# Optimization experiments

Hardware: AMD Instinct MI355X
Metric: run time of the kernel (lower is better)

## Reference

```python
import jax, jax.numpy as jnp
import numpy as np

N_NODES = 40000
N_EDGES = 320000
N_GRAPHS = 64
IN_DIM = 128
HID4 = 256   # hidden_dim * 4
OUT_DIM = 128
LN_EPS = 1e-5


def setup_inputs() -> dict:
    key = jax.random.key(0)
    ks = jax.random.split(key, 12)
    x = jax.random.normal(ks[0], (N_NODES, IN_DIM), dtype=jnp.float32)
    w = jax.random.uniform(ks[1], (N_EDGES, 4), dtype=jnp.float32)
    src = jax.random.randint(ks[2], (N_EDGES,), 0, N_NODES, dtype=jnp.int32)
    dst = jax.random.randint(ks[3], (N_EDGES,), 0, N_NODES, dtype=jnp.int32)
    graph_ids = jnp.sort(jax.random.randint(ks[4], (N_NODES,), 0, N_GRAPHS, dtype=jnp.int32))
    # parameters (no biases on GraphConv / fc1 linear)
    W1 = jax.random.normal(ks[5], (IN_DIM, HID4), dtype=jnp.float32) / np.sqrt(IN_DIM)
    fc1_W = jax.random.normal(ks[6], (IN_DIM, HID4), dtype=jnp.float32) / np.sqrt(IN_DIM)
    ln_gamma = jnp.ones((HID4,), dtype=jnp.float32)
    ln_beta = jnp.zeros((HID4,), dtype=jnp.float32)
    W2 = jax.random.normal(ks[7], (2 * HID4, HID4), dtype=jnp.float32) / np.sqrt(2 * HID4)
    W3 = jax.random.normal(ks[8], (HID4, OUT_DIM), dtype=jnp.float32) / np.sqrt(HID4)
    return {"x": x, "w": w, "W1": W1, "fc1_W": fc1_W, "ln_gamma": ln_gamma,
            "ln_beta": ln_beta, "W2": W2, "W3": W3,
            "src": src, "dst": dst, "graph_ids": graph_ids}


def _graph_conv(feat, src, dst, ew, W, out_inv_sqrt, in_inv_sqrt):
    # DGL GraphConv, norm='both', bias=False, with scalar edge_weight:
    # h = D_out^{-1/2} x ; m_e = w_e * h[src] ; agg = scatter_add(m, dst) ;
    # out = (D_in^{-1/2} agg) @ W
    h = feat * out_inv_sqrt[:, None]
    m = h[src] * ew[:, None]                       # [E, D] messages
    agg = jax.ops.segment_sum(m, dst, num_segments=N_NODES)
    return (agg * in_inv_sqrt[:, None]) @ W


def reference(x, w, W1, fc1_W, ln_gamma, ln_beta, W2, W3, src, dst, graph_ids):
    # unweighted degree normalization (DGL uses structural degrees, clamp(min=1))
    ones_e = jnp.ones((N_EDGES,), dtype=x.dtype)
    out_deg = jnp.maximum(jax.ops.segment_sum(ones_e, src, num_segments=N_NODES), 1.0)
    in_deg = jnp.maximum(jax.ops.segment_sum(ones_e, dst, num_segments=N_NODES), 1.0)
    out_inv = out_deg ** -0.5
    in_inv = in_deg ** -0.5

    ew = jnp.max(w, axis=1)                        # [E]

    x1 = jax.nn.relu(_graph_conv(x, src, dst, ew, W1, out_inv, in_inv))

    # fc1: Linear(no bias) -> LayerNorm(affine) -> ReLU
    f1 = x @ fc1_W
    mu = jnp.mean(f1, axis=-1, keepdims=True)
    var = jnp.mean((f1 - mu) ** 2, axis=-1, keepdims=True)
    f1 = (f1 - mu) * jax.lax.rsqrt(var + LN_EPS) * ln_gamma + ln_beta
    f1 = jax.nn.relu(f1)

    x1f1 = jnp.concatenate([x1, f1], axis=1)       # [N, 512]
    x2 = jax.nn.relu(_graph_conv(x1f1, src, dst, ew, W2, out_inv, in_inv))
    x3 = jax.nn.relu(_graph_conv(x2, src, dst, ew, W3, out_inv, in_inv))

    # dgl.sum_nodes over batched graph, then row-wise L2 normalize
    readout = jax.ops.segment_sum(x3, graph_ids, num_segments=N_GRAPHS)  # [G, OUT_DIM]
    norm = jnp.maximum(jnp.linalg.norm(readout, axis=1, keepdims=True), 1e-12)
    return readout / norm
```

## Files before the change

### kernel.cpp

```cpp
#include <hip/hip_runtime.h>

#define N_NODES 40000
#define M_PAD   40064
#define N_EDGES 320000
#define N_GRAPHS 64
#define IN_DIM 128
#define HID4 256
#define OUT_DIM 128
#define LN_EPS 1e-5f

typedef short  s16x8  __attribute__((ext_vector_type(8)));
typedef short  s16x4  __attribute__((ext_vector_type(4)));
typedef __bf16 bf16x8 __attribute__((ext_vector_type(8)));
typedef float  f32x4  __attribute__((ext_vector_type(4)));

__device__ __forceinline__ unsigned short f2b(float f) {
    unsigned int u = __builtin_bit_cast(unsigned int, f);
    u += 0x7fffu + ((u >> 16) & 1u);
    return (unsigned short)(u >> 16);
}
__device__ __forceinline__ float b2f(unsigned short h) {
    unsigned int u = (unsigned int)h << 16;
    return __builtin_bit_cast(float, u);
}

__device__ __forceinline__ void gll16(const unsigned short* g, short* lds_base) {
    __builtin_amdgcn_global_load_lds(
        (const __attribute__((address_space(1))) unsigned int*)g,
        (__attribute__((address_space(3))) unsigned int*)lds_base, 16, 0, 0);
}


#define XN (N_NODES * IN_DIM)
#define WN 229376
#define PREP_TOT (XN + WN + N_EDGES)

__global__ void prep_all(const float* __restrict__ x, const float* __restrict__ W1,
                         const float* __restrict__ fc1, const float* __restrict__ W2,
                         const float* __restrict__ W3, const float* __restrict__ w,
                         const int* __restrict__ src, const int* __restrict__ dst,
                         unsigned short* __restrict__ xb, unsigned short* __restrict__ W1t,
                         unsigned short* __restrict__ fc1t, unsigned short* __restrict__ W2t,
                         unsigned short* __restrict__ W3t, float* __restrict__ ew,
                         int* __restrict__ cnt_out, int* __restrict__ cnt_in) {
    int idx = blockIdx.x * 256 + threadIdx.x;
    if (idx < XN) { xb[idx] = f2b(x[idx]); return; }
    int j = idx - XN;
    if (j < 32768) { int k = j >> 8, n = j & 255; W1t[n * 128 + k] = f2b(W1[j]); return; }
    j -= 32768;
    if (j < 32768) { int k = j >> 8, n = j & 255; fc1t[n * 128 + k] = f2b(fc1[j]); return; }
    j -= 32768;
    if (j < 131072) { int k = j >> 8, n = j & 255; W2t[n * 512 + k] = f2b(W2[j]); return; }
    j -= 131072;
    if (j < 32768) { int k = j >> 7, n = j & 127; W3t[n * 256 + k] = f2b(W3[j]); return; }
    j -= 32768;
    if (j < N_EDGES) {
        float4 v = ((const float4*)w)[j];
        ew[j] = fmaxf(fmaxf(v.x, v.y), fmaxf(v.z, v.w));
        atomicAdd(&cnt_out[src[j]], 1);
        atomicAdd(&cnt_in[dst[j]], 1);
    }
}

__global__ void scan_part(const int* __restrict__ cnt, int* __restrict__ partial) {
    int b = blockIdx.x;
    int s = 0;
    for (int i = threadIdx.x; i < 1000; i += 256) s += cnt[b * 1000 + i];
#pragma unroll
    for (int m = 1; m < 64; m <<= 1) s += __shfl_xor(s, m);
    __shared__ int wsm[4];
    if ((threadIdx.x & 63) == 0) wsm[threadIdx.x >> 6] = s;
    __syncthreads();
    if (threadIdx.x == 0) partial[b] = wsm[0] + wsm[1] + wsm[2] + wsm[3];
}

__global__ void scan_final(const int* __restrict__ cnt_in, const int* __restrict__ cnt_out,
                           const int* __restrict__ partial, int* __restrict__ off,
                           float* __restrict__ out_inv, float* __restrict__ in_inv) {
    int b = blockIdx.x, tid = threadIdx.x;
    int lane = tid & 63, wv = tid >> 6;
    int pre = 0;
    for (int j = 0; j < b; ++j) pre += partial[j];
    int i = b * 1000 + tid;
    int v = (tid < 1000) ? cnt_in[i] : 0;
    int x = v;
#pragma unroll
    for (int ofs = 1; ofs < 64; ofs <<= 1) {
        int t = __shfl_up(x, ofs);
        if (lane >= ofs) x += t;
    }
    __shared__ int wsum[16];
    if (lane == 63) wsum[wv] = x;
    __syncthreads();
    if (wv == 0 && lane < 16) {
        int s = wsum[lane];
#pragma unroll
        for (int ofs = 1; ofs < 16; ofs <<= 1) {
            int t = __shfl_up(s, ofs);
            if (lane >= ofs) s += t;
        }
        wsum[lane] = s;
    }
    __syncthreads();
    int incl = pre + (wv > 0 ? wsum[wv - 1] : 0) + x;
    if (tid < 1000) {
        off[i] = incl - v;
        in_inv[i] = rsqrtf(fmaxf((float)v, 1.0f));
        out_inv[i] = rsqrtf(fmaxf((float)cnt_out[i], 1.0f));
    }
    if (b == 39 && tid == 999) off[N_NODES] = incl;
}

__global__ void csr_fill(const int* __restrict__ src, const int* __restrict__ dst,
                         const float* __restrict__ ew, const float* __restrict__ out_inv,
                         const int* __restrict__ off, int* __restrict__ cnt_in,
                         int2* __restrict__ es1, int2* __restrict__ es23) {
    int e = blockIdx.x * 256 + threadIdx.x;
    if (e >= N_EDGES) return;
    int d = dst[e];
    int slot = off[d] + atomicSub(&cnt_in[d], 1) - 1;
    int s = src[e];
    float wv = ew[e];
    es1[slot] = make_int2(s, __float_as_int(wv * out_inv[s]));
    es23[slot] = make_int2(s, __float_as_int(wv));
}


template <int D, int RELU>
__global__ void gather_nodes(const unsigned short* __restrict__ h, const int* __restrict__ off,
                             const int2* __restrict__ eg, const float* __restrict__ scale,
                             unsigned short* __restrict__ outb) {
    int n = blockIdx.x;
    int t = threadIdx.x;
    int b = off[n], e = off[n + 1];
    const unsigned int* hu = (const unsigned int*)h;
    float a0 = 0.0f, a1 = 0.0f;
    int i = b;
    for (; i + 3 < e; i += 4) {
        int2 e0 = eg[i], e1 = eg[i + 1], e2 = eg[i + 2], e3 = eg[i + 3];
        unsigned int p0 = hu[(size_t)e0.x * (D / 2) + t];
        unsigned int p1 = hu[(size_t)e1.x * (D / 2) + t];
        unsigned int p2 = hu[(size_t)e2.x * (D / 2) + t];
        unsigned int p3 = hu[(size_t)e3.x * (D / 2) + t];
        float w0 = __int_as_float(e0.y), w1 = __int_as_float(e1.y);
        float w2 = __int_as_float(e2.y), w3 = __int_as_float(e3.y);
        a0 += w0 * b2f((unsigned short)p0) + w1 * b2f((unsigned short)p1)
            + w2 * b2f((unsigned short)p2) + w3 * b2f((unsigned short)p3);
        a1 += w0 * b2f((unsigned short)(p0 >> 16)) + w1 * b2f((unsigned short)(p1 >> 16))
            + w2 * b2f((unsigned short)(p2 >> 16)) + w3 * b2f((unsigned short)(p3 >> 16));
    }
    for (; i < e; ++i) {
        int2 ee = eg[i];
        unsigned int p = hu[(size_t)ee.x * (D / 2) + t];
        float w0 = __int_as_float(ee.y);
        a0 += w0 * b2f((unsigned short)p);
        a1 += w0 * b2f((unsigned short)(p >> 16));
    }
    float sc = scale[n];
    a0 *= sc; a1 *= sc;
    if (RELU) { a0 = fmaxf(a0, 0.0f); a1 = fmaxf(a1, 0.0f); }
    unsigned int o = (unsigned int)f2b(a0) | ((unsigned int)f2b(a1) << 16);
    ((unsigned int*)outb)[(size_t)n * (D / 2) + t] = o;
}


__device__ __forceinline__ void gemm_core(short* As, short* Bs,
    const unsigned short* __restrict__ A, const unsigned short* __restrict__ A2,
    const unsigned short* __restrict__ Bt, unsigned short* __restrict__ C,
    const float* __restrict__ rowScaleC, int K1, int K2, int N,
    int relu, int scaleC, int m0, int n0) {
    int tid = threadIdx.x;
    int lane = tid & 63, wave = tid >> 6;
    int wm = (wave >> 1) * 64, wn = (wave & 1) * 64;
    int quad = lane >> 4, r16 = lane & 15;
    const int K = K1 + K2;
    f32x4 acc[4][4] = {};
    int lrow = wave * 16 + (lane >> 2);
    int kc = (lane & 3) * 8;
    short* ldsA = As + wave * 512;
    short* ldsB = Bs + wave * 512;

    for (int k0 = 0; k0 < K; k0 += 32) {
        int kk = k0 + kc;
#pragma unroll
        for (int h = 0; h < 2; ++h) {
            int r = h * 64 + lrow;
            const unsigned short* Ap = (kk < K1)
                ? A  + (size_t)(m0 + r) * K1 + kk
                : A2 + (size_t)(m0 + r) * K2 + (kk - K1);
            gll16(Ap, ldsA + h * 2048);
            gll16(Bt + (size_t)(n0 + r) * K + kk, ldsB + h * 2048);
        }
        __syncthreads();
        s16x8 af[4], bfr[4];
#pragma unroll
        for (int i = 0; i < 4; ++i)
            af[i] = *(const s16x8*)(As + (wm + i * 16 + r16) * 32 + quad * 8);
#pragma unroll
        for (int j = 0; j < 4; ++j)
            bfr[j] = *(const s16x8*)(Bs + (wn + j * 16 + r16) * 32 + quad * 8);
#pragma unroll
        for (int i = 0; i < 4; ++i)
#pragma unroll
            for (int j = 0; j < 4; ++j)
                acc[i][j] = __builtin_amdgcn_mfma_f32_16x16x32_bf16(
                    __builtin_bit_cast(bf16x8, af[i]), __builtin_bit_cast(bf16x8, bfr[j]),
                    acc[i][j], 0, 0, 0);
        __syncthreads();
    }

#pragma unroll
    for (int i = 0; i < 4; ++i) {
        int mbase = m0 + wm + i * 16 + quad * 4;
#pragma unroll
        for (int r = 0; r < 4; ++r) {
            int m = mbase + r;
            float sc = scaleC ? rowScaleC[m] : 1.0f;
#pragma unroll
            for (int j = 0; j < 4; ++j) {
                float v = acc[i][j][r] * sc;
                if (relu) v = fmaxf(v, 0.0f);
                C[(size_t)m * N + n0 + wn + j * 16 + r16] = f2b(v);
            }
        }
    }
}

template <int RELU, int SCALE_C>
__global__ __launch_bounds__(256) void gemm_mfma(
    const unsigned short* __restrict__ A, const unsigned short* __restrict__ A2,
    const unsigned short* __restrict__ Bt, unsigned short* __restrict__ C,
    const float* __restrict__ rowScaleC, int K1, int K2, int N) {
    __shared__ short As[4096];
    __shared__ short Bs[4096];
    gemm_core(As, Bs, A, A2, Bt, C, rowScaleC, K1, K2, N, RELU, SCALE_C,
              blockIdx.x * 128, blockIdx.y * 128);
}

__global__ __launch_bounds__(256) void gemm_dual(
    const unsigned short* __restrict__ A0, const unsigned short* __restrict__ B0,
    unsigned short* __restrict__ C0,
    const unsigned short* __restrict__ A1, const unsigned short* __restrict__ B1,
    unsigned short* __restrict__ C1) {
    __shared__ short As[4096];
    __shared__ short Bs[4096];
    const unsigned short* A  = blockIdx.z ? A1 : A0;
    const unsigned short* Bt = blockIdx.z ? B1 : B0;
    unsigned short* C        = blockIdx.z ? C1 : C0;
    gemm_core(As, Bs, A, A, Bt, C, nullptr, 128, 0, 256, blockIdx.z == 0, 0,
              blockIdx.x * 128, blockIdx.y * 128);
}


__global__ void ln_relu_bf16(unsigned short* __restrict__ f, const float* __restrict__ gamma,
                             const float* __restrict__ beta) {
    int row = (blockIdx.x * 256 + threadIdx.x) >> 6;
    int lane = threadIdx.x & 63;
    if (row >= N_NODES) return;
    s16x4* fr = (s16x4*)(f + (size_t)row * HID4);
    s16x4 pv = fr[lane];
    float v0 = b2f((unsigned short)pv[0]);
    float v1 = b2f((unsigned short)pv[1]);
    float v2 = b2f((unsigned short)pv[2]);
    float v3 = b2f((unsigned short)pv[3]);
    float sum = v0 + v1 + v2 + v3;
#pragma unroll
    for (int m = 1; m < 64; m <<= 1) sum += __shfl_xor(sum, m);
    float mu = sum * (1.0f / HID4);
    float d0 = v0 - mu, d1 = v1 - mu, d2 = v2 - mu, d3 = v3 - mu;
    float sq = d0 * d0 + d1 * d1 + d2 * d2 + d3 * d3;
#pragma unroll
    for (int m = 1; m < 64; m <<= 1) sq += __shfl_xor(sq, m);
    float rs = rsqrtf(sq * (1.0f / HID4) + LN_EPS);
    int c = lane * 4;
    s16x4 ov;
    ov[0] = (short)f2b(fmaxf(d0 * rs * gamma[c + 0] + beta[c + 0], 0.0f));
    ov[1] = (short)f2b(fmaxf(d1 * rs * gamma[c + 1] + beta[c + 1], 0.0f));
    ov[2] = (short)f2b(fmaxf(d2 * rs * gamma[c + 2] + beta[c + 2], 0.0f));
    ov[3] = (short)f2b(fmaxf(d3 * rs * gamma[c + 3] + beta[c + 3], 0.0f));
    fr[lane] = ov;
}


#define RO_NPB 16

__global__ void readout_sum(const unsigned short* __restrict__ x3, const int* __restrict__ gid,
                            float* __restrict__ ro) {
    int d = threadIdx.x;
    int n0 = blockIdx.x * RO_NPB;
    int n1 = n0 + RO_NPB;
    if (n1 > N_NODES) n1 = N_NODES;
    float acc = 0.0f;
    int cur = gid[n0];
    for (int n = n0; n < n1; ++n) {
        int g = gid[n];
        if (g != cur) {
            atomicAdd(&ro[cur * OUT_DIM + d], acc);
            acc = 0.0f;
            cur = g;
        }
        acc += b2f(x3[(size_t)n * OUT_DIM + d]);
    }
    atomicAdd(&ro[cur * OUT_DIM + d], acc);
}

__global__ void normalize_out(const float* __restrict__ ro, float* __restrict__ out) {
    int g = blockIdx.x;
    int d = threadIdx.x;
    float v = ro[g * OUT_DIM + d];
    float ss = v * v;
#pragma unroll
    for (int m = 1; m < 64; m <<= 1) ss += __shfl_xor(ss, m);
    __shared__ float s2[2];
    if ((d & 63) == 0) s2[d >> 6] = ss;
    __syncthreads();
    float tot = s2[0] + s2[1];
    float norm = fmaxf(sqrtf(tot), 1e-12f);
    out[g * OUT_DIM + d] = v / norm;
}


extern "C" void kernel_launch(void* const* d_in, const int* in_sizes, int n_in,
                              void* d_out, int out_size, void* d_ws, size_t ws_size,
                              hipStream_t stream) {
    const float* x    = (const float*)d_in[0];
    const float* w    = (const float*)d_in[1];
    const float* W1   = (const float*)d_in[2];
    const float* fc1W = (const float*)d_in[3];
    const float* gam  = (const float*)d_in[4];
    const float* bet  = (const float*)d_in[5];
    const float* W2   = (const float*)d_in[6];
    const float* W3   = (const float*)d_in[7];
    const int* src = (const int*)d_in[8];
    const int* dst = (const int*)d_in[9];
    const int* gid = (const int*)d_in[10];
    float* out = (float*)d_out;

    float* ws = (float*)d_ws;
    float* out_inv = ws + 0;
    float* in_inv  = ws + 40000;
    float* ew      = ws + 80000;
    int*   cnt_out = (int*)(ws + 400000);
    int*   cnt_in  = (int*)(ws + 440000);
    float* ro      = ws + 480000;
    unsigned short* W1t  = (unsigned short*)(ws + 488192);
    unsigned short* fc1t = (unsigned short*)(ws + 504576);
    unsigned short* W2t  = (unsigned short*)(ws + 520960);
    unsigned short* W3t  = (unsigned short*)(ws + 586496);
    int*   partial = (int*)(ws + 602880);
    int*   off     = (int*)(ws + 602920);
    int2*  es1     = (int2*)(ws + 642922);
    int2*  es23    = (int2*)(ws + 1282922);
    unsigned short* xb    = (unsigned short*)(ws + 1923000);
    unsigned short* Q3b   = xb;
    unsigned short* agg1b = (unsigned short*)(ws + 4487100);
    unsigned short* x2b   = agg1b;
    unsigned short* x1b   = (unsigned short*)(ws + 9615300);
    unsigned short* x3b   = x1b;
    unsigned short* f1b   = (unsigned short*)(ws + 14743500);
    unsigned short* P2b   = (unsigned short*)(ws + 19871700);

    hipMemsetAsync(cnt_out, 0, (2 * 40000 + N_GRAPHS * OUT_DIM) * sizeof(float), stream);

    prep_all<<<(PREP_TOT + 255) / 256, 256, 0, stream>>>(x, W1, fc1W, W2, W3, w, src, dst,
                                                         xb, W1t, fc1t, W2t, W3t, ew,
                                                         cnt_out, cnt_in);
    scan_part<<<40, 256, 0, stream>>>(cnt_in, partial);
    scan_final<<<40, 1024, 0, stream>>>(cnt_in, cnt_out, partial, off, out_inv, in_inv);
    csr_fill<<<(N_EDGES + 255) / 256, 256, 0, stream>>>(src, dst, ew, out_inv, off, cnt_in,
                                                        es1, es23);

    gather_nodes<IN_DIM, 0><<<N_NODES, IN_DIM / 2, 0, stream>>>(xb, off, es1, in_inv, agg1b);
    {
        dim3 grid(M_PAD / 128, HID4 / 128, 2);
        gemm_dual<<<grid, 256, 0, stream>>>(agg1b, W1t, x1b, xb, fc1t, f1b);
    }
    ln_relu_bf16<<<N_NODES / 4, 256, 0, stream>>>(f1b, gam, bet);

    {
        dim3 grid(M_PAD / 128, HID4 / 128);
        gemm_mfma<0, 1><<<grid, 256, 0, stream>>>(x1b, f1b, W2t, P2b, out_inv,
                                                  HID4, HID4, HID4);
    }
    gather_nodes<HID4, 1><<<N_NODES, HID4 / 2, 0, stream>>>(P2b, off, es23, in_inv, x2b);

    {
        dim3 grid(M_PAD / 128, OUT_DIM / 128);
        gemm_mfma<0, 1><<<grid, 256, 0, stream>>>(x2b, nullptr, W3t, Q3b, out_inv,
                                                  HID4, 0, OUT_DIM);
    }
    gather_nodes<OUT_DIM, 1><<<N_NODES, OUT_DIM / 2, 0, stream>>>(Q3b, off, es23, in_inv, x3b);

    readout_sum<<<(N_NODES + RO_NPB - 1) / RO_NPB, 128, 0, stream>>>(x3b, gid, ro);
    normalize_out<<<N_GRAPHS, 128, 0, stream>>>(ro, out);
}
```

Before: 298.3 us.

## Fuse LayerNorm into fc1 GEMM epilogue and layer-3 gather into readout

The dual GEMM now covers the full 256-column width per block with 512 threads, so the LayerNorm row statistics for fc1 can be reduced in shared memory and applied in the epilogue. This removes the separate ln_relu pass over f1. The layer-3 gather also feeds the per-graph readout directly with atomics, so x3 is never written out or re-read. The costs are fewer GEMM blocks, a single-pass variance formula (E[x²]−mu²) that can lose precision, and a gather kernel that handles 8 nodes per 64-thread block and may expose less parallelism.

```diff
diff --git a/kernel.cpp b/kernel.cpp
--- a/kernel.cpp
+++ b/kernel.cpp
@@ -10,7 +10,6 @@
 #define LN_EPS 1e-5f
 
 typedef short  s16x8  __attribute__((ext_vector_type(8)));
-typedef short  s16x4  __attribute__((ext_vector_type(4)));
 typedef __bf16 bf16x8 __attribute__((ext_vector_type(8)));
 typedef float  f32x4  __attribute__((ext_vector_type(4)));
 
@@ -164,6 +163,58 @@
 }
 
 
+#define G3_NPB 8
+
+__global__ void gather3_ro(const unsigned short* __restrict__ h, const int* __restrict__ off,
+                           const int2* __restrict__ eg, const float* __restrict__ scale,
+                           const int* __restrict__ gid, float* __restrict__ ro) {
+    int t = threadIdx.x;
+    int n0 = blockIdx.x * G3_NPB;
+    int n1 = n0 + G3_NPB;
+    if (n1 > N_NODES) n1 = N_NODES;
+    const unsigned int* hu = (const unsigned int*)h;
+    float r0 = 0.0f, r1 = 0.0f;
+    int cur = gid[n0];
+    for (int n = n0; n < n1; ++n) {
+        int g = gid[n];
+        if (g != cur) {
+            atomicAdd(&ro[cur * OUT_DIM + 2 * t], r0);
+            atomicAdd(&ro[cur * OUT_DIM + 2 * t + 1], r1);
+            r0 = r1 = 0.0f;
+            cur = g;
+        }
+        int b = off[n], e = off[n + 1];
+        float a0 = 0.0f, a1 = 0.0f;
+        int i = b;
+        for (; i + 3 < e; i += 4) {
+            int2 e0 = eg[i], e1 = eg[i + 1], e2 = eg[i + 2], e3 = eg[i + 3];
+            unsigned int p0 = hu[(size_t)e0.x * 64 + t];
+            unsigned int p1 = hu[(size_t)e1.x * 64 + t];
+            unsigned int p2 = hu[(size_t)e2.x * 64 + t];
+            unsigned int p3 = hu[(size_t)e3.x * 64 + t];
+            float w0 = __int_as_float(e0.y), w1 = __int_as_float(e1.y);
+            float w2 = __int_as_float(e2.y), w3 = __int_as_float(e3.y);
+            a0 += w0 * b2f((unsigned short)p0) + w1 * b2f((unsigned short)p1)
+                + w2 * b2f((unsigned short)p2) + w3 * b2f((unsigned short)p3);
+            a1 += w0 * b2f((unsigned short)(p0 >> 16)) + w1 * b2f((unsigned short)(p1 >> 16))
+                + w2 * b2f((unsigned short)(p2 >> 16)) + w3 * b2f((unsigned short)(p3 >> 16));
+        }
+        for (; i < e; ++i) {
+            int2 ee = eg[i];
+            unsigned int p = hu[(size_t)ee.x * 64 + t];
+            float w0 = __int_as_float(ee.y);
+            a0 += w0 * b2f((unsigned short)p);
+            a1 += w0 * b2f((unsigned short)(p >> 16));
+        }
+        float sc = scale[n];
+        r0 += fmaxf(a0 * sc, 0.0f);
+        r1 += fmaxf(a1 * sc, 0.0f);
+    }
+    atomicAdd(&ro[cur * OUT_DIM + 2 * t], r0);
+    atomicAdd(&ro[cur * OUT_DIM + 2 * t + 1], r1);
+}
+
+
 __device__ __forceinline__ void gemm_core(short* As, short* Bs,
     const unsigned short* __restrict__ A, const unsigned short* __restrict__ A2,
     const unsigned short* __restrict__ Bt, unsigned short* __restrict__ C,
@@ -237,72 +288,106 @@
               blockIdx.x * 128, blockIdx.y * 128);
 }
 
-__global__ __launch_bounds__(256) void gemm_dual(
+
+__global__ __launch_bounds__(512) void gemm_dual(
     const unsigned short* __restrict__ A0, const unsigned short* __restrict__ B0,
     unsigned short* __restrict__ C0,
     const unsigned short* __restrict__ A1, const unsigned short* __restrict__ B1,
-    unsigned short* __restrict__ C1) {
+    unsigned short* __restrict__ C1,
+    const float* __restrict__ gamma, const float* __restrict__ beta) {
     __shared__ short As[4096];
-    __shared__ short Bs[4096];
+    __shared__ short Bs[8192];
+    __shared__ float lns[128][4];
+    __shared__ float lnq[128][4];
     const unsigned short* A  = blockIdx.z ? A1 : A0;
     const unsigned short* Bt = blockIdx.z ? B1 : B0;
     unsigned short* C        = blockIdx.z ? C1 : C0;
-    gemm_core(As, Bs, A, A, Bt, C, nullptr, 128, 0, 256, blockIdx.z == 0, 0,
-              blockIdx.x * 128, blockIdx.y * 128);
-}
-
-
-__global__ void ln_relu_bf16(unsigned short* __restrict__ f, const float* __restrict__ gamma,
-                             const float* __restrict__ beta) {
-    int row = (blockIdx.x * 256 + threadIdx.x) >> 6;
-    int lane = threadIdx.x & 63;
-    if (row >= N_NODES) return;
-    s16x4* fr = (s16x4*)(f + (size_t)row * HID4);
-    s16x4 pv = fr[lane];
-    float v0 = b2f((unsigned short)pv[0]);
-    float v1 = b2f((unsigned short)pv[1]);
-    float v2 = b2f((unsigned short)pv[2]);
-    float v3 = b2f((unsigned short)pv[3]);
-    float sum = v0 + v1 + v2 + v3;
-#pragma unroll
-    for (int m = 1; m < 64; m <<= 1) sum += __shfl_xor(sum, m);
-    float mu = sum * (1.0f / HID4);
-    float d0 = v0 - mu, d1 = v1 - mu, d2 = v2 - mu, d3 = v3 - mu;
-    float sq = d0 * d0 + d1 * d1 + d2 * d2 + d3 * d3;
-#pragma unroll
-    for (int m = 1; m < 64; m <<= 1) sq += __shfl_xor(sq, m);
-    float rs = rsqrtf(sq * (1.0f / HID4) + LN_EPS);
-    int c = lane * 4;
-    s16x4 ov;
-    ov[0] = (short)f2b(fmaxf(d0 * rs * gamma[c + 0] + beta[c + 0], 0.0f));
-    ov[1] = (short)f2b(fmaxf(d1 * rs * gamma[c + 1] + beta[c + 1], 0.0f));
-    ov[2] = (short)f2b(fmaxf(d2 * rs * gamma[c + 2] + beta[c + 2], 0.0f));
-    ov[3] = (short)f2b(fmaxf(d3 * rs * gamma[c + 3] + beta[c + 3], 0.0f));
-    fr[lane] = ov;
-}
-
-
-#define RO_NPB 16
-
-__global__ void readout_sum(const unsigned short* __restrict__ x3, const int* __restrict__ gid,
-                            float* __restrict__ ro) {
-    int d = threadIdx.x;
-    int n0 = blockIdx.x * RO_NPB;
-    int n1 = n0 + RO_NPB;
-    if (n1 > N_NODES) n1 = N_NODES;
-    float acc = 0.0f;
-    int cur = gid[n0];
-    for (int n = n0; n < n1; ++n) {
-        int g = gid[n];
-        if (g != cur) {
-            atomicAdd(&ro[cur * OUT_DIM + d], acc);
-            acc = 0.0f;
-            cur = g;
-        }
-        acc += b2f(x3[(size_t)n * OUT_DIM + d]);
-    }
-    atomicAdd(&ro[cur * OUT_DIM + d], acc);
-}
+    int tid = threadIdx.x;
+    int lane = tid & 63, wave = tid >> 6;
+    int wm = (wave >> 2) * 64, wn = (wave & 3) * 64;
+    int quad = lane >> 4, r16 = lane & 15;
+    int m0 = blockIdx.x * 128;
+    f32x4 acc[4][4] = {};
+    int lrow = lane >> 2;
+    int kc = (lane & 3) * 8;
+    short* ldsA = As + wave * 512;
+    short* ldsB = Bs + wave * 512;
+
+    for (int k0 = 0; k0 < 128; k0 += 32) {
+        int kk = k0 + kc;
+        int rr = wave * 16 + lrow;
+        gll16(A + (size_t)(m0 + rr) * 128 + kk, ldsA);
+        gll16(Bt + (size_t)rr * 128 + kk, ldsB);
+        gll16(Bt + (size_t)(128 + rr) * 128 + kk, ldsB + 4096);
+        __syncthreads();
+        s16x8 af[4], bfr[4];
+#pragma unroll
+        for (int i = 0; i < 4; ++i)
+            af[i] = *(const s16x8*)(As + (wm + i * 16 + r16) * 32 + quad * 8);
+#pragma unroll
+        for (int j = 0; j < 4; ++j)
+            bfr[j] = *(const s16x8*)(Bs + (wn + j * 16 + r16) * 32 + quad * 8);
+#pragma unroll
+        for (int i = 0; i < 4; ++i)
+#pragma unroll
+            for (int j = 0; j < 4; ++j)
+                acc[i][j] = __builtin_amdgcn_mfma_f32_16x16x32_bf16(
+                    __builtin_bit_cast(bf16x8, af[i]), __builtin_bit_cast(bf16x8, bfr[j]),
+                    acc[i][j], 0, 0, 0);
+        __syncthreads();
+    }
+
+    if (blockIdx.z == 0) {
+#pragma unroll
+        for (int i = 0; i < 4; ++i) {
+            int mbase = m0 + wm + i * 16 + quad * 4;
+#pragma unroll
+            for (int r = 0; r < 4; ++r) {
+                int m = mbase + r;
+#pragma unroll
+                for (int j = 0; j < 4; ++j)
+                    C[(size_t)m * 256 + wn + j * 16 + r16] = f2b(fmaxf(acc[i][j][r], 0.0f));
+            }
+        }
+    } else {
+#pragma unroll
+        for (int i = 0; i < 4; ++i)
+#pragma unroll
+            for (int r = 0; r < 4; ++r) {
+                float s = 0.0f, q = 0.0f;
+#pragma unroll
+                for (int j = 0; j < 4; ++j) { float v = acc[i][j][r]; s += v; q += v * v; }
+#pragma unroll
+                for (int m = 1; m < 16; m <<= 1) { s += __shfl_xor(s, m); q += __shfl_xor(q, m); }
+                if (r16 == 0) {
+                    int row = wm + i * 16 + quad * 4 + r;
+                    lns[row][wave & 3] = s;
+                    lnq[row][wave & 3] = q;
+                }
+            }
+        __syncthreads();
+#pragma unroll
+        for (int i = 0; i < 4; ++i) {
+#pragma unroll
+            for (int r = 0; r < 4; ++r) {
+                int row = wm + i * 16 + quad * 4 + r;
+                float s = lns[row][0] + lns[row][1] + lns[row][2] + lns[row][3];
+                float q = lnq[row][0] + lnq[row][1] + lnq[row][2] + lnq[row][3];
+                float mu = s * (1.0f / HID4);
+                float var = q * (1.0f / HID4) - mu * mu;
+                float rs = rsqrtf(var + LN_EPS);
+                int m = m0 + row;
+#pragma unroll
+                for (int j = 0; j < 4; ++j) {
+                    int col = wn + j * 16 + r16;
+                    float v = (acc[i][j][r] - mu) * rs * gamma[col] + beta[col];
+                    C[(size_t)m * 256 + col] = f2b(fmaxf(v, 0.0f));
+                }
+            }
+        }
+    }
+}
+
 
 __global__ void normalize_out(const float* __restrict__ ro, float* __restrict__ out) {
     int g = blockIdx.x;
@@ -356,7 +441,6 @@
     unsigned short* agg1b = (unsigned short*)(ws + 4487100);
     unsigned short* x2b   = agg1b;
     unsigned short* x1b   = (unsigned short*)(ws + 9615300);
-    unsigned short* x3b   = x1b;
     unsigned short* f1b   = (unsigned short*)(ws + 14743500);
     unsigned short* P2b   = (unsigned short*)(ws + 19871700);
 
@@ -372,10 +456,9 @@
 
     gather_nodes<IN_DIM, 0><<<N_NODES, IN_DIM / 2, 0, stream>>>(xb, off, es1, in_inv, agg1b);
     {
-        dim3 grid(M_PAD / 128, HID4 / 128, 2);
-        gemm_dual<<<grid, 256, 0, stream>>>(agg1b, W1t, x1b, xb, fc1t, f1b);
-    }
-    ln_relu_bf16<<<N_NODES / 4, 256, 0, stream>>>(f1b, gam, bet);
+        dim3 grid(M_PAD / 128, 1, 2);
+        gemm_dual<<<grid, 512, 0, stream>>>(agg1b, W1t, x1b, xb, fc1t, f1b, gam, bet);
+    }
 
     {
         dim3 grid(M_PAD / 128, HID4 / 128);
@@ -389,8 +472,7 @@
         gemm_mfma<0, 1><<<grid, 256, 0, stream>>>(x2b, nullptr, W3t, Q3b, out_inv,
                                                   HID4, 0, OUT_DIM);
     }
-    gather_nodes<OUT_DIM, 1><<<N_NODES, OUT_DIM / 2, 0, stream>>>(Q3b, off, es23, in_inv, x3b);
-
-    readout_sum<<<(N_NODES + RO_NPB - 1) / RO_NPB, 128, 0, stream>>>(x3b, gid, ro);
+    gather3_ro<<<(N_NODES + G3_NPB - 1) / G3_NPB, 64, 0, stream>>>(Q3b, off, es23, in_inv,
+                                                                   gid, ro);
     normalize_out<<<N_GRAPHS, 128, 0, stream>>>(ro, out);
 }
```

Result: faster. 285.6 us (-4.3%).
